# Performance work log

Measured on AMD Instinct MI355X. Metric: run time of the kernel, lower is better.

Reference implementation:

```python
import jax, jax.numpy as jnp
import numpy as np

N = 4096        # batch nodes
E = 65536       # random edges (self-loops appended -> 69632 total)
F_IN = 256
H = 128
C = 2
MIN = 1024      # minority (class 1) count; first MIN nodes
REP = 2         # int(N_pct/100) synthetic reps per minority sample


def setup_inputs() -> dict:
    key = jax.random.key(0)
    ks = jax.random.split(key, 24)
    feat = jax.random.normal(ks[0], (N, F_IN), dtype=jnp.float32)
    src = jax.random.randint(ks[1], (E,), 0, N, dtype=jnp.int32)
    dst = jax.random.randint(ks[2], (E,), 0, N, dtype=jnp.int32)
    loops = jnp.arange(N, dtype=jnp.int32)
    src = jnp.concatenate([src, loops])
    dst = jnp.concatenate([dst, loops])
    # dense batch adjacency (target for EdgeLoss), A[i,j]=1 if edge j->i
    adj = jnp.zeros((N, N), dtype=jnp.float32).at[dst, src].set(1.0)
    # deterministic labels: first MIN nodes are minority class 1
    labels = jnp.concatenate([jnp.ones((MIN,), jnp.int32), jnp.zeros((N - MIN,), jnp.int32)])

    def w(k, shape, fan_in):
        return jax.random.normal(k, shape, dtype=jnp.float32) / np.sqrt(fan_in)

    params = dict(
        W_pool0=w(ks[3], (F_IN, F_IN), F_IN), b_pool0=jnp.zeros((F_IN,), jnp.float32),
        W_self0=w(ks[4], (H, F_IN), F_IN), W_neigh0=w(ks[5], (H, F_IN), F_IN), b0=jnp.zeros((H,), jnp.float32),
        W_pool1=w(ks[6], (H, H), H), b_pool1=jnp.zeros((H,), jnp.float32),
        W_self1=w(ks[7], (H, H), H), W_neigh1=w(ks[8], (H, H), H), b1=jnp.zeros((H,), jnp.float32),
        de_weight=jax.random.uniform(ks[9], (H, H), jnp.float32, -1.0 / np.sqrt(H), 1.0 / np.sqrt(H)),
        W_conv=w(ks[10], (H, 2 * H), 2 * H),
        W_clf=w(ks[11], (C, H), H), b_clf=jnp.zeros((C,), jnp.float32),
        gaps=jax.random.uniform(ks[12], (MIN, REP), jnp.float32),  # SMOTE interpolation gaps
    )
    return dict(feat=feat, adj=adj, src=src, dst=dst, labels=labels, **params)


def _sage_pool_layer(h, src, dst, W_pool, b_pool, W_self, W_neigh, b):
    # DGL SAGEConv aggregator_type='pool': max over neighbors of relu(fc_pool(h))
    p = jax.nn.relu(h @ W_pool.T + b_pool)                     # [N, d]
    hn = jax.ops.segment_max(p[src], dst, num_segments=h.shape[0])
    hn = jnp.where(jnp.isfinite(hn), hn, 0.0)
    return h @ W_self.T + hn @ W_neigh.T + b


def _l2norm(x, eps=1e-12):
    return x / jnp.maximum(jnp.linalg.norm(x, axis=1, keepdims=True), eps)


def _smote_nn_interp(cand, gaps):
    # pairwise euclidean distances (vectorized form of the per-row loop)
    sq = jnp.sum(cand * cand, axis=1)
    d2 = sq[:, None] + sq[None, :] - 2.0 * (cand @ cand.T)
    dist = jnp.sqrt(jnp.maximum(d2, 0.0))
    nn_idx = jnp.argsort(dist, axis=1)[:, 1]                   # k=2 -> single nearest (excl. self)
    diff = cand[nn_idx] - cand                                  # [MIN, H]
    synth = cand[:, None, :] + gaps[:, :, None] * diff[:, None, :]  # [MIN, REP, H], i-major order
    return synth.reshape(MIN * REP, cand.shape[1])


def reference(feat, adj, src, dst, labels,
              W_pool0, b_pool0, W_self0, W_neigh0, b0,
              W_pool1, b_pool1, W_self1, W_neigh1, b1,
              de_weight, W_conv, W_clf, b_clf, gaps):
    # ---- Encoder (2 SAGEConv 'pool' layers; dropout is eval-mode identity) ----
    h = _sage_pool_layer(feat, src, dst, W_pool0, b_pool0, W_self0, W_neigh0, b0)
    h = _l2norm(jax.nn.relu(h))
    h = _sage_pool_layer(h, src, dst, W_pool1, b_pool1, W_self1, W_neigh1, b1)
    # ---- SMOTE (minority = first MIN rows, by deterministic label construction) ----
    synth = _smote_nn_interp(h[:MIN], gaps)
    x = jnp.concatenate([h, synth], axis=0)                    # [N + MIN*REP, H]
    y = jnp.concatenate([labels, jnp.ones((MIN * REP,), jnp.int32)])
    # ---- Decoder: sigmoid(out @ out.T) ----
    out = x @ de_weight.T
    pred_adj = jax.nn.sigmoid(out @ out.T)                     # [6144, 6144]
    # ---- EdgeLoss vs dense batch adjacency ----
    rec = pred_adj[:N, :N]
    edge_num = jnp.sum(adj != 0).astype(jnp.float32)
    neg_w = edge_num / (float(N * N) - edge_num)
    weight = jnp.where(adj == 0, neg_w, 1.0)
    loss = jnp.sum(weight * (rec - adj) ** 2)
    # ---- threshold + SageClassifier (1 layer, no activation before clf) ----
    pred_adj = jnp.where(pred_adj >= 0.5, pred_adj, 0.0)
    neigh = (pred_adj @ x) / (jnp.sum(pred_adj, axis=1, keepdims=True) + 1.0)
    hc = jnp.concatenate([x, neigh], axis=-1) @ W_conv.T
    logits = hc @ W_clf.T + b_clf                              # [6144, 2]
    return logits, y, loss
```

## Files before the change

kernel.cpp:

```cpp
#include <hip/hip_runtime.h>
#include <cstddef>

typedef unsigned short ushort_t;
typedef __attribute__((ext_vector_type(8))) short bf16x8;
typedef __attribute__((ext_vector_type(4))) float f32x4;
typedef __attribute__((ext_vector_type(16))) float f32x16;

#define WS_P0     0u
#define WS_DOTS   0u
#define WS_OBK    524288u
#define WS_HN0    1048576u
#define WS_H1     2097152u
#define WS_H1N    2621440u
#define WS_P1     3145728u
#define WS_PVB    3145728u
#define WS_HN1    3670016u
#define WS_H2     4194304u
#define WS_X      4718592u
#define WS_BITMAP 5767168u
#define WS_NEIGH  6291456u
#define WS_ROWSUM 7077888u
#define WS_SCAL   7084032u
#define WS_DEG    7084048u
#define WS_NN     7088144u
#define WS_CUR    7089168u
#define WS_ROWPTR 7093264u
#define WS_EIDX   7097361u

__device__ inline ushort_t f2bf(float f) {
  unsigned u = __float_as_uint(f);
  u += 0x7fff + ((u >> 16) & 1);
  return (ushort_t)(u >> 16);
}
__device__ inline float bf2f(ushort_t h) {
  return __uint_as_float((unsigned)h << 16);
}

__global__ __launch_bounds__(256, 2) void mgemm(
    const float* __restrict__ A, int lda,
    const float* __restrict__ B, int ldb,
    const float* __restrict__ A2, int lda2,
    const float* __restrict__ B2, int ldb2,
    const float* __restrict__ bias,
    float* __restrict__ C, int ldc,
    int K, int relu,
    ushort_t* __restrict__ Cb,
    const float* __restrict__ a2scale,
    const float* __restrict__ Ahi,
    int cbplain,
    const float* __restrict__ Wclf,
    const float* __restrict__ scal4,
    float* __restrict__ outp)
{
  __shared__ ushort_t AhS[64][36], AlS[64][36], BhS[64][36], BlS[64][36];
  const int tid = threadIdx.x;
  const int lane = tid & 63;
  const int w = tid >> 6;
  const int lo = lane & 31, hi = lane >> 5;
  const int iq = (w & 1) << 5, jq = (w >> 1) << 5;
  const int i0 = blockIdx.y << 6, j0 = blockIdx.x << 6;
  const int lr = tid >> 2;
  const int c8 = (tid & 3) << 3;
  f32x16 acc;
#pragma unroll
  for (int t = 0; t < 16; ++t) acc[t] = 0.f;
  const int npass = (A2 != nullptr) ? 2 : 1;
  for (int pass = 0; pass < npass; ++pass) {
    const float* Ap = pass ? A2 : A; const int la = pass ? lda2 : lda;
    const float* Bp = pass ? B2 : B; const int lb = pass ? ldb2 : ldb;
    const float* Arow = (pass == 0 && Ahi != nullptr && (i0 + lr) >= 4096)
        ? (Ahi + (size_t)(i0 + lr - 4096) * la)
        : (Ap + (size_t)(i0 + lr) * la);
    const float* Brow = Bp + (size_t)(j0 + lr) * lb;
    const float sc = (pass && a2scale) ? __frcp_rn(a2scale[i0 + lr] + 1.f) : 1.f;
    for (int k0 = 0; k0 < K; k0 += 32) {
      float av[8], bv[8];
      {
        const float4 a0 = *(const float4*)(Arow + k0 + c8);
        const float4 a1 = *(const float4*)(Arow + k0 + c8 + 4);
        const float4 b0 = *(const float4*)(Brow + k0 + c8);
        const float4 b1 = *(const float4*)(Brow + k0 + c8 + 4);
        av[0]=a0.x*sc; av[1]=a0.y*sc; av[2]=a0.z*sc; av[3]=a0.w*sc;
        av[4]=a1.x*sc; av[5]=a1.y*sc; av[6]=a1.z*sc; av[7]=a1.w*sc;
        bv[0]=b0.x; bv[1]=b0.y; bv[2]=b0.z; bv[3]=b0.w;
        bv[4]=b1.x; bv[5]=b1.y; bv[6]=b1.z; bv[7]=b1.w;
      }
      __syncthreads();
      {
        ushort_t ah8[8], al8[8], bh8[8], bl8[8];
#pragma unroll
        for (int e = 0; e < 8; ++e) {
          const ushort_t ah = f2bf(av[e]);
          ah8[e] = ah; al8[e] = f2bf(av[e] - bf2f(ah));
          const ushort_t bh = f2bf(bv[e]);
          bh8[e] = bh; bl8[e] = f2bf(bv[e] - bf2f(bh));
        }
        *(bf16x8*)&AhS[lr][c8] = *(bf16x8*)ah8;
        *(bf16x8*)&AlS[lr][c8] = *(bf16x8*)al8;
        *(bf16x8*)&BhS[lr][c8] = *(bf16x8*)bh8;
        *(bf16x8*)&BlS[lr][c8] = *(bf16x8*)bl8;
      }
      __syncthreads();
#pragma unroll
      for (int kk = 0; kk < 32; kk += 16) {
        const bf16x8 ahf = *(const bf16x8*)&AhS[iq + lo][kk + (hi << 3)];
        const bf16x8 alf = *(const bf16x8*)&AlS[iq + lo][kk + (hi << 3)];
        const bf16x8 bhf = *(const bf16x8*)&BhS[jq + lo][kk + (hi << 3)];
        const bf16x8 blf = *(const bf16x8*)&BlS[jq + lo][kk + (hi << 3)];
        acc = __builtin_amdgcn_mfma_f32_32x32x16_bf16(ahf, bhf, acc, 0, 0, 0);
        acc = __builtin_amdgcn_mfma_f32_32x32x16_bf16(alf, bhf, acc, 0, 0, 0);
        acc = __builtin_amdgcn_mfma_f32_32x32x16_bf16(ahf, blf, acc, 0, 0, 0);
      }
    }
  }
  const int col = j0 + jq + lo;
  if (Wclf) {
    const float w0c = Wclf[col], w1c = Wclf[128 + col];
#pragma unroll
    for (int t = 0; t < 16; ++t) {
      float q0 = acc[t] * w0c, q1 = acc[t] * w1c;
#pragma unroll
      for (int m = 1; m < 32; m <<= 1) {
        q0 += __shfl_xor(q0, m, 64);
        q1 += __shfl_xor(q1, m, 64);
      }
      if (lo == 0) {
        const int row = i0 + iq + (t & 3) + ((t >> 2) << 3) + (hi << 2);
        atomicAdd(&outp[(size_t)row * 2 + 0], q0);
        atomicAdd(&outp[(size_t)row * 2 + 1], q1);
      }
    }
    if (blockIdx.x == 0 && blockIdx.y == 0 && tid == 0) {
      const float cnt = scal4[4];
      const float neg_w = cnt / (16777216.f - cnt);
      outp[18432] = neg_w * (scal4[0] - scal4[3]) + scal4[1];
    }
    return;
  }
  const float badd = bias ? bias[col] : 0.f;
#pragma unroll
  for (int t = 0; t < 16; ++t) {
    float o = acc[t] + badd;
    if (relu) o = fmaxf(o, 0.f);
    const int row = i0 + iq + (t & 3) + ((t >> 2) << 3) + (hi << 2);
    if (Cb) {
      if (cbplain) {
        Cb[(size_t)row * ldc + col] = f2bf(o);
      } else {
        const size_t off = ((size_t)(row >> 5) << 12) +
            (size_t)(((col >> 4) << 9) +
                     (((((col >> 3) & 1) << 5) + (row & 31)) << 3) + (col & 7));
        Cb[off] = f2bf(o);
      }
    } else {
      C[(size_t)row * ldc + col] = o;
    }
  }
}

__global__ void count_bitmap_k(const int* __restrict__ src, const int* __restrict__ dst,
                               int* __restrict__ deg, unsigned* __restrict__ bitmap, int E) {
  const int e = blockIdx.x * 256 + threadIdx.x;
  if (e < E) {
    const int d_ = dst[e], s_ = src[e];
    atomicAdd(&deg[d_], 1);
    const unsigned cell = ((unsigned)d_ << 12) + (unsigned)s_;
    atomicOr(&bitmap[cell >> 5], 1u << (cell & 31));
  }
}

__global__ __launch_bounds__(1024) void scan_k(const int* __restrict__ deg,
                                               int* __restrict__ rowptr,
                                               int* __restrict__ cursor) {
  __shared__ int sums[1024];
  const int t = threadIdx.x;
  const int4 d = *(const int4*)(deg + (t << 2));
  const int local = d.x + d.y + d.z + d.w;
  sums[t] = local;
  __syncthreads();
  for (int off = 1; off < 1024; off <<= 1) {
    int v = (t >= off) ? sums[t - off] : 0;
    __syncthreads();
    sums[t] += v;
    __syncthreads();
  }
  const int excl = sums[t] - local;
  const int o0 = excl, o1 = o0 + d.x, o2 = o1 + d.y, o3 = o2 + d.z;
  rowptr[(t<<2)+0]=o0; rowptr[(t<<2)+1]=o1; rowptr[(t<<2)+2]=o2; rowptr[(t<<2)+3]=o3;
  cursor[(t<<2)+0]=o0; cursor[(t<<2)+1]=o1; cursor[(t<<2)+2]=o2; cursor[(t<<2)+3]=o3;
  if (t == 1023) rowptr[4096] = sums[1023];
}

__global__ void fill_k(const int* __restrict__ src, const int* __restrict__ dst,
                       int* __restrict__ cursor, int* __restrict__ eidx, int E) {
  const int e = blockIdx.x * 256 + threadIdx.x;
  if (e < E) {
    const int p = atomicAdd(&cursor[dst[e]], 1);
    eidx[p] = src[e];
  }
}

__global__ void segmax_bf_k(const ushort_t* __restrict__ p, const int* __restrict__ rowptr,
                            const int* __restrict__ eidx, float* __restrict__ hn, int F) {
  const int row = blockIdx.x, f = threadIdx.x;
  const int b = rowptr[row], e = rowptr[row + 1];
  float m = 0.f;
  for (int k = b; k < e; ++k) m = fmaxf(m, bf2f(p[(size_t)eidx[k] * F + f]));
  hn[(size_t)row * F + f] = m;
}

__device__ inline float wave_sum(float v) {
#pragma unroll
  for (int o = 32; o > 0; o >>= 1) v += __shfl_down(v, o, 64);
  return v;
}

__global__ void relu_l2norm_k(const float* __restrict__ in, float* __restrict__ out) {
  const int row = blockIdx.x, f = threadIdx.x;
  const float v = fmaxf(in[(size_t)row * 128 + f], 0.f);
  const float ss = wave_sum(v * v);
  __shared__ float w[2];
  if ((f & 63) == 0) w[f >> 6] = ss;
  __syncthreads();
  const float denom = fmaxf(sqrtf(w[0] + w[1]), 1e-12f);
  out[(size_t)row * 128 + f] = v / denom;
}

__global__ void argmin_k(const float* __restrict__ dots, int* __restrict__ nn) {
  __shared__ float sqd[1024];
  const int i = blockIdx.x, tid = threadIdx.x;
#pragma unroll
  for (int z = 0; z < 4; ++z) {
    const int j = (tid << 2) + z;
    sqd[j] = dots[(size_t)j * 1025];
  }
  __syncthreads();
  float best = 3.402823466e38f; int bidx = 0x7fffffff;
  const float si = sqd[i];
  for (int j = tid; j < 1024; j += 256) {
    if (j == i) continue;
    float d2 = si + sqd[j] - 2.f * dots[(size_t)i * 1024 + j];
    d2 = fmaxf(d2, 0.f);
    if (d2 < best || (d2 == best && j < bidx)) { best = d2; bidx = j; }
  }
  __shared__ float bv[256]; __shared__ int bi[256];
  bv[tid] = best; bi[tid] = bidx;
  __syncthreads();
  for (int s = 128; s > 0; s >>= 1) {
    if (tid < s) {
      if (bv[tid+s] < bv[tid] || (bv[tid+s] == bv[tid] && bi[tid+s] < bi[tid])) {
        bv[tid] = bv[tid+s]; bi[tid] = bi[tid+s];
      }
    }
    __syncthreads();
  }
  if (tid == 0) nn[i] = bi[0];
}

__global__ __launch_bounds__(256) void build_pack_k(
    const float* __restrict__ h2, const int* __restrict__ nn,
    const float* __restrict__ gaps, float* __restrict__ synth,
    ushort_t* __restrict__ pvb,
    const int* __restrict__ labels, const float* __restrict__ bclf,
    float* __restrict__ outp) {
  __shared__ ushort_t s[4096];
  const int jt = blockIdx.x, tid = threadIdx.x;
  if (tid < 32) {
    const int i = (jt << 5) + tid;
    outp[(size_t)i * 2 + 0] = bclf[0];
    outp[(size_t)i * 2 + 1] = bclf[1];
    outp[12288 + i] = (i < 4096) ? (float)labels[i] : 1.f;
  }
  if (jt < 128) {
    const float* ip = h2 + ((size_t)jt << 12);
#pragma unroll
    for (int k = 0; k < 4; ++k) {
      const float4 v = *(const float4*)(ip + (tid << 4) + (k << 2));
      ushort4 h; h.x = f2bf(v.x); h.y = f2bf(v.y); h.z = f2bf(v.z); h.w = f2bf(v.w);
      *(ushort4*)(s + (tid << 4) + (k << 2)) = h;
    }
  } else {
    const int row = tid >> 3;
    const int sIdx = ((jt - 128) << 5) + row;
    const int i = sIdx >> 1;
    const float g = gaps[sIdx];
    const int ni = nn[i];
#pragma unroll
    for (int k = 0; k < 4; ++k) {
      const int f = ((tid & 7) << 4) + (k << 2);
      const float4 c4 = *(const float4*)(h2 + (size_t)i * 128 + f);
      const float4 n4 = *(const float4*)(h2 + (size_t)ni * 128 + f);
      float4 v;
      v.x = c4.x + g * (n4.x - c4.x);
      v.y = c4.y + g * (n4.y - c4.y);
      v.z = c4.z + g * (n4.z - c4.z);
      v.w = c4.w + g * (n4.w - c4.w);
      *(float4*)(synth + (size_t)sIdx * 128 + f) = v;
      ushort4 h; h.x = f2bf(v.x); h.y = f2bf(v.y); h.z = f2bf(v.z); h.w = f2bf(v.w);
      *(ushort4*)(s + (row << 7) + f) = h;
    }
  }
  __syncthreads();
  const int u = tid & 31, ft = (tid >> 5) & 3, cc = tid >> 7;
  ushort_t* op = pvb + ((size_t)jt << 12) + (cc << 11) + (ft << 9);
#pragma unroll
  for (int m = 0; m < 2; ++m) {
    const int l = (u << 1) + m;
    const int f = (ft << 5) + (l & 31);
    const int jb = (cc << 4) + ((l >> 5) << 3);
    ushort4 o0, o1;
    o0.x = s[(jb + 0) * 128 + f]; o0.y = s[(jb + 1) * 128 + f];
    o0.z = s[(jb + 2) * 128 + f]; o0.w = s[(jb + 3) * 128 + f];
    o1.x = s[(jb + 4) * 128 + f]; o1.y = s[(jb + 5) * 128 + f];
    o1.z = s[(jb + 6) * 128 + f]; o1.w = s[(jb + 7) * 128 + f];
    *(ushort4*)(op + (l << 3) + 0) = o0;
    *(ushort4*)(op + (l << 3) + 4) = o1;
  }
}

__global__ __launch_bounds__(256, 2) void fused_mfma(
    const ushort_t* __restrict__ obk,
    const ushort_t* __restrict__ pvb,
    const unsigned* __restrict__ bitmap,
    float* __restrict__ neigh,
    float* __restrict__ rowsum,
    float* __restrict__ scal)
{
  __shared__ float wred[4][4];
  const int tid = threadIdx.x;
  const int w = tid >> 6;
  const int lane = tid & 63;
  const int lo = lane & 31, hi = lane >> 5;
  const int it = (blockIdx.x << 2) + w;
  const int iw = it << 5;
  const int jt0 = blockIdx.y << 4;
  const bool loss_i = (it < 128);

  bf16x8 qf[8];
  {
    const ushort_t* qp = obk + ((size_t)it << 12) + (lane << 3);
#pragma unroll
    for (int c = 0; c < 8; ++c) qf[c] = *(const bf16x8*)(qp + (c << 9));
  }
  f32x16 oacc[4];
#pragma unroll
  for (int ft = 0; ft < 4; ++ft)
#pragma unroll
    for (int r = 0; r < 16; ++r) oacc[ft][r] = 0.f;
  float rs = 0.f, s_all = 0.f, s1a = 0.f, suba = 0.f, ecf = 0.f;

  bf16x8 a[8];
  {
    const ushort_t* kp = obk + ((size_t)jt0 << 12) + (lane << 3);
#pragma unroll
    for (int c = 0; c < 8; ++c) a[c] = *(const bf16x8*)(kp + (c << 9));
  }

  for (int t = 0; t < 16; ++t) {
    const int jt = jt0 + t;
    f32x16 s0, s1;
#pragma unroll
    for (int r = 0; r < 16; ++r) { s0[r] = 0.f; s1[r] = 0.f; }
#pragma unroll
    for (int c = 0; c < 4; ++c) {
      s0 = __builtin_amdgcn_mfma_f32_32x32x16_bf16(a[c], qf[c], s0, 0, 0, 0);
      s1 = __builtin_amdgcn_mfma_f32_32x32x16_bf16(a[c + 4], qf[c + 4], s1, 0, 0, 0);
    }
    bf16x8 bvf[2][4];
    {
      const ushort_t* vp = pvb + ((size_t)jt << 12) + (lane << 3);
#pragma unroll
      for (int cc = 0; cc < 2; ++cc)
#pragma unroll
        for (int ft = 0; ft < 4; ++ft)
          bvf[cc][ft] = *(const bf16x8*)(vp + (cc << 11) + (ft << 9));
    }
    if (t < 15) {
      const ushort_t* kp = obk + ((size_t)(jt + 1) << 12) + (lane << 3);
#pragma unroll
      for (int c = 0; c < 8; ++c) a[c] = *(const bf16x8*)(kp + (c << 9));
    }
    const bool loss_t = loss_i && (jt < 128);
    unsigned word = 0u;
    if (loss_t) word = bitmap[((unsigned)(iw + lo) << 7) + (unsigned)jt];
    float p[16];
    if (loss_t) {
      ecf += (float)__popc(word & (0x0F0F0F0Fu << (hi << 2)));
#pragma unroll
      for (int r = 0; r < 16; ++r) {
        const float v = s0[r] + s1[r];
        const float sg = __builtin_amdgcn_rcpf(1.f + __expf(-v));
        const int jl = (r & 3) + ((r >> 2) << 3) + (hi << 2);
        const float e_ = (float)((word >> jl) & 1u);
        s_all += sg * sg;
        s1a  += e_ * (sg - 1.f) * (sg - 1.f);
        suba += e_ * sg * sg;
        const float tv = (v >= 0.f) ? sg : 0.f;
        p[r] = tv; rs += tv;
      }
    } else {
#pragma unroll
      for (int r = 0; r < 16; ++r) {
        const float v = s0[r] + s1[r];
        const float sg = __builtin_amdgcn_rcpf(1.f + __expf(-v));
        const float tv = (v >= 0.f) ? sg : 0.f;
        p[r] = tv; rs += tv;
      }
    }
#pragma unroll
    for (int cc = 0; cc < 2; ++cc) {
      const int b8 = cc << 3;
      unsigned c01, c23, c45, c67;
      asm("v_cvt_pk_bf16_f32 %0, %1, %2" : "=v"(c01) : "v"(p[b8+0]), "v"(p[b8+1]));
      asm("v_cvt_pk_bf16_f32 %0, %1, %2" : "=v"(c23) : "v"(p[b8+2]), "v"(p[b8+3]));
      asm("v_cvt_pk_bf16_f32 %0, %1, %2" : "=v"(c45) : "v"(p[b8+4]), "v"(p[b8+5]));
      asm("v_cvt_pk_bf16_f32 %0, %1, %2" : "=v"(c67) : "v"(p[b8+6]), "v"(p[b8+7]));
      const auto w0 = __builtin_amdgcn_permlane32_swap((int)c01, (int)c45, false, false);
      const auto w1 = __builtin_amdgcn_permlane32_swap((int)c23, (int)c67, false, false);
      union { int i[4]; bf16x8 h; } u;
      u.i[0] = w0[0]; u.i[1] = w1[0]; u.i[2] = w0[1]; u.i[3] = w1[1];
#pragma unroll
      for (int ft = 0; ft < 4; ++ft)
        oacc[ft] = __builtin_amdgcn_mfma_f32_32x32x16_bf16(u.h, bvf[cc][ft], oacc[ft], 0, 0, 0);
    }
  }
#pragma unroll
  for (int ft = 0; ft < 4; ++ft)
#pragma unroll
    for (int r = 0; r < 16; ++r) {
      const int ir = (r & 3) + ((r >> 2) << 3) + (hi << 2);
      atomicAdd(&neigh[(size_t)(iw + ir) * 128 + (ft << 5) + lo], oacc[ft][r]);
    }
  rs += __shfl_xor(rs, 32, 64);
  if (hi == 0) atomicAdd(&rowsum[iw + lo], rs);
  {
    float v0 = wave_sum(s_all), v1 = wave_sum(s1a), v2 = wave_sum(suba), v3 = wave_sum(ecf);
    if (lane == 0) { wred[w][0] = v0; wred[w][1] = v1; wred[w][2] = v2; wred[w][3] = v3; }
  }
  __syncthreads();
  if (tid < 4) {
    const float t = wred[0][tid] + wred[1][tid] + wred[2][tid] + wred[3][tid];
    const int dst = (tid == 0) ? 0 : (tid == 1) ? 1 : (tid == 2) ? 3 : 4;
    atomicAdd(&scal[dst], t);
  }
}

extern "C" void kernel_launch(void* const* d_in, const int* in_sizes, int n_in,
                              void* d_out, int out_size, void* d_ws, size_t ws_size,
                              hipStream_t stream) {
  const float* feat     = (const float*)d_in[0];
  const int*   src      = (const int*)d_in[2];
  const int*   dst      = (const int*)d_in[3];
  const int*   labels   = (const int*)d_in[4];
  const float* W_pool0  = (const float*)d_in[5];
  const float* b_pool0  = (const float*)d_in[6];
  const float* W_self0  = (const float*)d_in[7];
  const float* W_neigh0 = (const float*)d_in[8];
  const float* b0       = (const float*)d_in[9];
  const float* W_pool1  = (const float*)d_in[10];
  const float* b_pool1  = (const float*)d_in[11];
  const float* W_self1  = (const float*)d_in[12];
  const float* W_neigh1 = (const float*)d_in[13];
  const float* b1       = (const float*)d_in[14];
  const float* de_w     = (const float*)d_in[15];
  const float* W_conv   = (const float*)d_in[16];
  const float* W_clf    = (const float*)d_in[17];
  const float* b_clf    = (const float*)d_in[18];
  const float* gaps     = (const float*)d_in[19];
  const int E = in_sizes[2];

  float* ws = (float*)d_ws;
  ushort_t* p0b   = (ushort_t*)(ws + WS_P0);
  float* dots     = ws + WS_DOTS;
  ushort_t* obk   = (ushort_t*)(ws + WS_OBK);
  float* hn0      = ws + WS_HN0;
  unsigned* bitmap= (unsigned*)(ws + WS_BITMAP);
  float* h1       = ws + WS_H1;
  float* h1n      = ws + WS_H1N;
  ushort_t* p1b   = (ushort_t*)(ws + WS_P1);
  ushort_t* pvb   = (ushort_t*)(ws + WS_PVB);
  float* hn1      = ws + WS_HN1;
  float* h2       = ws + WS_H2;
  float* synth    = ws + WS_X;
  float* neigh    = ws + WS_NEIGH;
  float* rowsum   = ws + WS_ROWSUM;
  float* scal     = ws + WS_SCAL;
  int* deg        = (int*)(ws + WS_DEG);
  int* nn         = (int*)(ws + WS_NN);
  int* cursor     = (int*)(ws + WS_CUR);
  int* rowptr     = (int*)(ws + WS_ROWPTR);
  int* eidx       = (int*)(ws + WS_EIDX);

  float* outp = (float*)d_out;
  const dim3 blk(256);

  hipMemsetAsync(bitmap, 0, (size_t)(WS_DEG + 4096 - WS_BITMAP) * 4, stream);

  count_bitmap_k<<<(E + 255) / 256, blk, 0, stream>>>(src, dst, deg, bitmap, E);
  scan_k<<<1, 1024, 0, stream>>>(deg, rowptr, cursor);
  fill_k<<<(E + 255) / 256, blk, 0, stream>>>(src, dst, cursor, eidx, E);

  mgemm<<<dim3(4, 64), blk, 0, stream>>>(feat, 256, W_pool0, 256,
                                         nullptr, 0, nullptr, 0,
                                         b_pool0, nullptr, 256, 256, 1, p0b, nullptr, nullptr,
                                         1, nullptr, nullptr, nullptr);
  segmax_bf_k<<<4096, 256, 0, stream>>>(p0b, rowptr, eidx, hn0, 256);
  mgemm<<<dim3(2, 64), blk, 0, stream>>>(feat, 256, W_self0, 256,
                                         hn0, 256, W_neigh0, 256,
                                         b0, h1, 128, 256, 0, nullptr, nullptr, nullptr,
                                         0, nullptr, nullptr, nullptr);
  relu_l2norm_k<<<4096, 128, 0, stream>>>(h1, h1n);

  mgemm<<<dim3(2, 64), blk, 0, stream>>>(h1n, 128, W_pool1, 128,
                                         nullptr, 0, nullptr, 0,
                                         b_pool1, nullptr, 128, 128, 1, p1b, nullptr, nullptr,
                                         1, nullptr, nullptr, nullptr);
  segmax_bf_k<<<4096, 128, 0, stream>>>(p1b, rowptr, eidx, hn1, 128);
  mgemm<<<dim3(2, 64), blk, 0, stream>>>(h1n, 128, W_self1, 128,
                                         hn1, 128, W_neigh1, 128,
                                         b1, h2, 128, 128, 0, nullptr, nullptr, nullptr,
                                         0, nullptr, nullptr, nullptr);

  mgemm<<<dim3(16, 16), blk, 0, stream>>>(h2, 128, h2, 128,
                                          nullptr, 0, nullptr, 0,
                                          nullptr, dots, 1024, 128, 0, nullptr, nullptr, nullptr,
                                          0, nullptr, nullptr, nullptr);
  argmin_k<<<1024, 256, 0, stream>>>(dots, nn);
  build_pack_k<<<192, blk, 0, stream>>>(h2, nn, gaps, synth, pvb, labels, b_clf, outp);

  mgemm<<<dim3(2, 96), blk, 0, stream>>>(h2, 128, de_w, 128,
                                         nullptr, 0, nullptr, 0,
                                         nullptr, nullptr, 0, 128, 0, obk, nullptr, synth,
                                         0, nullptr, nullptr, nullptr);
  fused_mfma<<<dim3(48, 12), blk, 0, stream>>>(obk, pvb, bitmap, neigh, rowsum, scal);

  mgemm<<<dim3(2, 96), blk, 0, stream>>>(h2, 128, W_conv, 256,
                                         neigh, 128, W_conv + 128, 256,
                                         nullptr, nullptr, 128, 128, 0, nullptr, rowsum, synth,
                                         0, W_clf, scal, outp);

  (void)n_in; (void)out_size; (void)ws_size; (void)in_sizes;
}
```

Measured before the change: 308.0 us.

## Store pool activations in fp32 and raise wave priority around MFMA blocks

```diff
diff --git a/kernel.cpp b/kernel.cpp
--- a/kernel.cpp
+++ b/kernel.cpp
@@ -47,7 +47,6 @@
     ushort_t* __restrict__ Cb,
     const float* __restrict__ a2scale,
     const float* __restrict__ Ahi,
-    int cbplain,
     const float* __restrict__ Wclf,
     const float* __restrict__ scal4,
     float* __restrict__ outp)
@@ -144,14 +143,10 @@
     if (relu) o = fmaxf(o, 0.f);
     const int row = i0 + iq + (t & 3) + ((t >> 2) << 3) + (hi << 2);
     if (Cb) {
-      if (cbplain) {
-        Cb[(size_t)row * ldc + col] = f2bf(o);
-      } else {
-        const size_t off = ((size_t)(row >> 5) << 12) +
-            (size_t)(((col >> 4) << 9) +
-                     (((((col >> 3) & 1) << 5) + (row & 31)) << 3) + (col & 7));
-        Cb[off] = f2bf(o);
-      }
+      const size_t off = ((size_t)(row >> 5) << 12) +
+          (size_t)(((col >> 4) << 9) +
+                   (((((col >> 3) & 1) << 5) + (row & 31)) << 3) + (col & 7));
+      Cb[off] = f2bf(o);
     } else {
       C[(size_t)row * ldc + col] = o;
     }
@@ -200,12 +195,12 @@
   }
 }
 
-__global__ void segmax_bf_k(const ushort_t* __restrict__ p, const int* __restrict__ rowptr,
-                            const int* __restrict__ eidx, float* __restrict__ hn, int F) {
+__global__ void segmax_k(const float* __restrict__ p, const int* __restrict__ rowptr,
+                         const int* __restrict__ eidx, float* __restrict__ hn, int F) {
   const int row = blockIdx.x, f = threadIdx.x;
   const int b = rowptr[row], e = rowptr[row + 1];
   float m = 0.f;
-  for (int k = b; k < e; ++k) m = fmaxf(m, bf2f(p[(size_t)eidx[k] * F + f]));
+  for (int k = b; k < e; ++k) m = fmaxf(m, p[(size_t)eidx[k] * F + f]);
   hn[(size_t)row * F + f] = m;
 }
 
@@ -361,11 +356,13 @@
     f32x16 s0, s1;
 #pragma unroll
     for (int r = 0; r < 16; ++r) { s0[r] = 0.f; s1[r] = 0.f; }
+    __builtin_amdgcn_s_setprio(1);
 #pragma unroll
     for (int c = 0; c < 4; ++c) {
       s0 = __builtin_amdgcn_mfma_f32_32x32x16_bf16(a[c], qf[c], s0, 0, 0, 0);
       s1 = __builtin_amdgcn_mfma_f32_32x32x16_bf16(a[c + 4], qf[c + 4], s1, 0, 0, 0);
     }
+    __builtin_amdgcn_s_setprio(0);
     bf16x8 bvf[2][4];
     {
       const ushort_t* vp = pvb + ((size_t)jt << 12) + (lane << 3);
@@ -419,9 +416,11 @@
       const auto w1 = __builtin_amdgcn_permlane32_swap((int)c23, (int)c67, false, false);
       union { int i[4]; bf16x8 h; } u;
       u.i[0] = w0[0]; u.i[1] = w1[0]; u.i[2] = w0[1]; u.i[3] = w1[1];
+      __builtin_amdgcn_s_setprio(1);
 #pragma unroll
       for (int ft = 0; ft < 4; ++ft)
         oacc[ft] = __builtin_amdgcn_mfma_f32_32x32x16_bf16(u.h, bvf[cc][ft], oacc[ft], 0, 0, 0);
+      __builtin_amdgcn_s_setprio(0);
     }
   }
 #pragma unroll
@@ -470,14 +469,14 @@
   const int E = in_sizes[2];
 
   float* ws = (float*)d_ws;
-  ushort_t* p0b   = (ushort_t*)(ws + WS_P0);
+  float* p0       = ws + WS_P0;
   float* dots     = ws + WS_DOTS;
   ushort_t* obk   = (ushort_t*)(ws + WS_OBK);
   float* hn0      = ws + WS_HN0;
   unsigned* bitmap= (unsigned*)(ws + WS_BITMAP);
   float* h1       = ws + WS_H1;
   float* h1n      = ws + WS_H1N;
-  ushort_t* p1b   = (ushort_t*)(ws + WS_P1);
+  float* p1       = ws + WS_P1;
   ushort_t* pvb   = (ushort_t*)(ws + WS_PVB);
   float* hn1      = ws + WS_HN1;
   float* h2       = ws + WS_H2;
@@ -502,42 +501,42 @@
 
   mgemm<<<dim3(4, 64), blk, 0, stream>>>(feat, 256, W_pool0, 256,
                                          nullptr, 0, nullptr, 0,
-                                         b_pool0, nullptr, 256, 256, 1, p0b, nullptr, nullptr,
-                                         1, nullptr, nullptr, nullptr);
-  segmax_bf_k<<<4096, 256, 0, stream>>>(p0b, rowptr, eidx, hn0, 256);
+                                         b_pool0, p0, 256, 256, 1, nullptr, nullptr, nullptr,
+                                         nullptr, nullptr, nullptr);
+  segmax_k<<<4096, 256, 0, stream>>>(p0, rowptr, eidx, hn0, 256);
   mgemm<<<dim3(2, 64), blk, 0, stream>>>(feat, 256, W_self0, 256,
                                          hn0, 256, W_neigh0, 256,
                                          b0, h1, 128, 256, 0, nullptr, nullptr, nullptr,
-                                         0, nullptr, nullptr, nullptr);
+                                         nullptr, nullptr, nullptr);
   relu_l2norm_k<<<4096, 128, 0, stream>>>(h1, h1n);
 
   mgemm<<<dim3(2, 64), blk, 0, stream>>>(h1n, 128, W_pool1, 128,
                                          nullptr, 0, nullptr, 0,
-                                         b_pool1, nullptr, 128, 128, 1, p1b, nullptr, nullptr,
-                                         1, nullptr, nullptr, nullptr);
-  segmax_bf_k<<<4096, 128, 0, stream>>>(p1b, rowptr, eidx, hn1, 128);
+                                         b_pool1, p1, 128, 128, 1, nullptr, nullptr, nullptr,
+                                         nullptr, nullptr, nullptr);
+  segmax_k<<<4096, 128, 0, stream>>>(p1, rowptr, eidx, hn1, 128);
   mgemm<<<dim3(2, 64), blk, 0, stream>>>(h1n, 128, W_self1, 128,
                                          hn1, 128, W_neigh1, 128,
                                          b1, h2, 128, 128, 0, nullptr, nullptr, nullptr,
-                                         0, nullptr, nullptr, nullptr);
+                                         nullptr, nullptr, nullptr);
 
   mgemm<<<dim3(16, 16), blk, 0, stream>>>(h2, 128, h2, 128,
                                           nullptr, 0, nullptr, 0,
                                           nullptr, dots, 1024, 128, 0, nullptr, nullptr, nullptr,
-                                          0, nullptr, nullptr, nullptr);
+                                          nullptr, nullptr, nullptr);
   argmin_k<<<1024, 256, 0, stream>>>(dots, nn);
   build_pack_k<<<192, blk, 0, stream>>>(h2, nn, gaps, synth, pvb, labels, b_clf, outp);
 
   mgemm<<<dim3(2, 96), blk, 0, stream>>>(h2, 128, de_w, 128,
                                          nullptr, 0, nullptr, 0,
                                          nullptr, nullptr, 0, 128, 0, obk, nullptr, synth,
-                                         0, nullptr, nullptr, nullptr);
+                                         nullptr, nullptr, nullptr);
   fused_mfma<<<dim3(48, 12), blk, 0, stream>>>(obk, pvb, bitmap, neigh, rowsum, scal);
 
   mgemm<<<dim3(2, 96), blk, 0, stream>>>(h2, 128, W_conv, 256,
                                          neigh, 128, W_conv + 128, 256,
                                          nullptr, nullptr, 128, 128, 0, nullptr, rowsum, synth,
-                                         0, W_clf, scal, outp);
+                                         W_clf, scal, outp);
 
   (void)n_in; (void)out_size; (void)ws_size; (void)in_sizes;
 }
```

Measured after the change: 306.2 us. No clear change (-0.6%).
